# Optimization experiments

Hardware: AMD Instinct MI355X
Metric: run time of the kernel (lower is better)

The kernel has to match this reference:

```python
import jax, jax.numpy as jnp
import numpy as np

NVOC = 50257
DIM = 256
HID = 256
NUM_LAYERS = 2
SEQ = 128
BATCH = 16


def setup_inputs() -> dict:
    key = jax.random.key(0)
    ks = jax.random.split(key, 16)
    u = 0.1
    inp = {
        "tokens": jax.random.randint(ks[0], (SEQ, BATCH), 0, NVOC),
        "emb": jax.random.uniform(ks[1], (NVOC, DIM), jnp.float32, -u, u),
        # gate weights are zero-initialized nn.Parameters in the original; use small
        # random values so gradients/activations are non-degenerate
        "wf": jax.random.normal(ks[2], (HID, HID), jnp.float32) * 0.05,
        "uf": jax.random.normal(ks[3], (DIM, HID), jnp.float32) * 0.05,
        "bf": jnp.zeros((HID,), jnp.float32),
        "wi": jax.random.normal(ks[4], (HID, HID), jnp.float32) * 0.05,
        "ui": jax.random.normal(ks[5], (DIM, HID), jnp.float32) * 0.05,
        "bi": jnp.zeros((HID,), jnp.float32),
        "wc": jax.random.normal(ks[6], (HID, HID), jnp.float32) * 0.05,
        "uc": jax.random.normal(ks[7], (DIM, HID), jnp.float32) * 0.05,
        "bc": jnp.zeros((HID,), jnp.float32),
        "wo": jax.random.normal(ks[8], (HID, HID), jnp.float32) * 0.05,
        "uo": jax.random.normal(ks[9], (DIM, HID), jnp.float32) * 0.05,
        "bo": jnp.zeros((HID,), jnp.float32),
        "dec_w": jax.random.uniform(ks[10], (NVOC, HID), jnp.float32, -u, u),
        "dec_b": jnp.zeros((NVOC,), jnp.float32),
    }
    return inp


def reference(tokens, emb, wf, uf, bf, wi, ui, bi, wc, uc, bc, wo, uo, bo,
              dec_w, dec_b):
    # embeddings: (T, B, D); dropout is identity (eval / p honored as 0)
    x_seq = emb[tokens]

    h0 = jnp.zeros((NUM_LAYERS, BATCH, HID), jnp.float32)
    c0 = jnp.zeros((NUM_LAYERS, BATCH, HID), jnp.float32)

    def step(carry, x_t):
        h, c = carry
        x = x_t  # (B, D)
        hs, cs = [], []
        for l in range(NUM_LAYERS):  # fixed small structural loop
            hp, cp = h[l], c[l]
            f = jax.nn.sigmoid(hp @ wf + x @ uf + bf)
            i = jax.nn.sigmoid(hp @ wi + x @ ui + bi)
            o = jax.nn.sigmoid(hp @ wo + x @ uo + bo)
            g = jnp.tanh(hp @ wc + x @ uc + bc)
            cn = f * cp + i * g
            hn = o * jnp.tanh(cn)
            hs.append(hn)
            cs.append(cn)
            x = hn  # next layer consumes this layer's hidden state
        return (jnp.stack(hs), jnp.stack(cs)), x  # emit top-layer h

    (hT, cT), h_top = jax.lax.scan(step, (h0, c0), x_seq)  # h_top: (T, B, H)
    logits = jnp.einsum('tbh,vh->tbv', h_top, dec_w) + dec_b  # (T, B, V)
    return logits, hT, cT
```

## Files before the change

### kernel.cpp

```cpp
#include <hip/hip_runtime.h>
#include <hip/hip_bf16.h>

#define NVOC 50257
#define DIM 256
#define HID 256
#define NLAYER 2
#define SEQ 128
#define BATCH 16
#define GUARD (1 << 20)
#define NCHUNK 197
#define DECBLKS (32 * NCHUNK)
#define FL_L0 0
#define FL_XV 16
#define FL_L1 32
#define FSTR 64

typedef __bf16 bf16x8 __attribute__((ext_vector_type(8)));
typedef float f32x4 __attribute__((ext_vector_type(4)));
typedef unsigned short u16;
typedef unsigned int u32;
typedef unsigned long long u64;

#define AL64(p)   __hip_atomic_load((const u64*)(p), __ATOMIC_RELAXED, __HIP_MEMORY_SCOPE_AGENT)
#define AS32(p,v) __hip_atomic_store((u32*)(p), (v), __ATOMIC_RELAXED, __HIP_MEMORY_SCOPE_AGENT)

__device__ __forceinline__ float fsig(float z) { return 1.f / (1.f + __expf(-z)); }
__device__ __forceinline__ float ftanh(float z) {
  const float x = fminf(fmaxf(z, -15.f), 15.f);
  const float e = __expf(2.f * x);
  return (e - 1.f) / (e + 1.f);
}
__device__ __forceinline__ bf16x8 cvt8(const float4 u0, const float4 u1) {
  bf16x8 v;
  v[0] = (__bf16)u0.x; v[1] = (__bf16)u0.y; v[2] = (__bf16)u0.z; v[3] = (__bf16)u0.w;
  v[4] = (__bf16)u1.x; v[5] = (__bf16)u1.y; v[6] = (__bf16)u1.z; v[7] = (__bf16)u1.w;
  return v;
}

__device__ __forceinline__ bool all16(const u32* fp) {
  const u64 m = AL64(fp) & AL64(fp + 2) & AL64(fp + 4) & AL64(fp + 6)
              & AL64(fp + 8) & AL64(fp + 10) & AL64(fp + 12) & AL64(fp + 14);
  return ((u32)m & (u32)(m >> 32)) != 0u;
}
__device__ __forceinline__ void pollwave(const u32* fp, int lane) {
  if (lane == 0) {
    int gd = 0;
    while (!all16(fp) && ++gd < GUARD) {}
  }
  asm volatile("" ::: "memory");
}

__global__ void zero_kernel(u32* __restrict__ flg) {
  for (int i = threadIdx.x; i < SEQ * FSTR; i += 256) AS32(&flg[i], 0u);
}

__global__ __launch_bounds__(256) void xu_kernel(
    const int* __restrict__ tokp, const float* __restrict__ embp,
    const float* __restrict__ uF, const float* __restrict__ uI,
    const float* __restrict__ uC, const float* __restrict__ uO,
    const float* __restrict__ bF, const float* __restrict__ bI,
    const float* __restrict__ bC, const float* __restrict__ bO,
    float* __restrict__ XU)
{
  const int tid = threadIdx.x;
  const int lane = tid & 63, wv = tid >> 6, r16 = lane & 15, kgrp = lane >> 4;
  const int m0 = blockIdx.x * 16;
  const int n0 = blockIdx.y * 256 + wv * 64;
  const float* Ug[4] = {uF, uI, uC, uO};
  const float* Bp[4] = {bF, bI, bC, bO};

  bf16x8 b[4][8];
  float bias[4];
#pragma unroll
  for (int nt = 0; nt < 4; ++nt) {
    const int n = n0 + nt * 16 + r16;
    const float* U = Ug[n >> 8];
    const int c = n & 255;
    bias[nt] = Bp[n >> 8][c];
#pragma unroll
    for (int kk = 0; kk < 8; ++kk) {
      const int kb = kk * 32 + kgrp * 8;
      bf16x8 v;
#pragma unroll
      for (int e = 0; e < 8; ++e) v[e] = (__bf16)U[(size_t)(kb + e) * HID + c];
      b[nt][kk] = v;
    }
  }

  const int tok = tokp[m0 + r16];
  const float* x = embp + (size_t)tok * DIM;
  bf16x8 a[8];
#pragma unroll
  for (int kk = 0; kk < 8; ++kk) {
    const int kb = kk * 32 + kgrp * 8;
    a[kk] = cvt8(*reinterpret_cast<const float4*>(x + kb),
                 *reinterpret_cast<const float4*>(x + kb + 4));
  }
#pragma unroll
  for (int nt = 0; nt < 4; ++nt) {
    f32x4 acc = {0.f, 0.f, 0.f, 0.f};
#pragma unroll
    for (int kk = 0; kk < 8; ++kk)
      acc = __builtin_amdgcn_mfma_f32_16x16x32_bf16(a[kk], b[nt][kk], acc, 0, 0, 0);
    const int n = n0 + nt * 16 + r16;
#pragma unroll
    for (int r = 0; r < 4; ++r)
      XU[(size_t)(m0 + kgrp * 4 + r) * 1024 + n] = acc[r] + bias[nt];
  }
}

__global__ __launch_bounds__(512, 1) void mega_kernel(
    const float* __restrict__ wF, const float* __restrict__ wI,
    const float* __restrict__ wC, const float* __restrict__ wO,
    const float* __restrict__ uF, const float* __restrict__ uI,
    const float* __restrict__ uC, const float* __restrict__ uO,
    const float* __restrict__ bF, const float* __restrict__ bI,
    const float* __restrict__ bC, const float* __restrict__ bO,
    const float* __restrict__ XU, float* __restrict__ V,
    u32* __restrict__ h0w, u32* __restrict__ h1w,
    u32* __restrict__ flg, const float* __restrict__ dw,
    const float* __restrict__ dbp, float* __restrict__ dout)
{
  const int tid  = threadIdx.x;
  const int lane = tid & 63;
  const int wv   = tid >> 6;
  const int r16  = lane & 15;
  const int kgrp = lane >> 4;
  const int bx   = blockIdx.x;

  if (bx >= 6) {
    const int db = bx - 6;
    const int mb = db / NCHUNK;
    const int nb = db - mb * NCHUNK;
    const int n0 = nb * 256 + wv * 32;

    bf16x8 b[2][8];
    float bb[2];
#pragma unroll
    for (int nt = 0; nt < 2; ++nt) {
      const int v = n0 + nt * 16 + r16;
      const int vc = (v < NVOC) ? v : (NVOC - 1);
      bb[nt] = dbp[vc];
      const float* bp = dw + (size_t)vc * HID + kgrp * 8;
#pragma unroll
      for (int kk = 0; kk < 8; ++kk)
        b[nt][kk] = cvt8(*reinterpret_cast<const float4*>(bp + kk * 32),
                         *reinterpret_cast<const float4*>(bp + kk * 32 + 4));
    }

    if (tid == 0) {
      const u32* fp = flg + (size_t)(mb * 4 + 3) * FSTR + FL_L1;
      int gd = 0;
      while (!all16(fp) && ++gd < GUARD) __builtin_amdgcn_s_sleep(64);
    }
    __syncthreads();

    const u16* htb = (const u16*)h1w;
    bf16x8 a[4][8];
#pragma unroll
    for (int mt = 0; mt < 4; ++mt) {
      const u16* ap = htb + ((size_t)(mb * 64 + mt * 16 + r16)) * HID + kgrp * 8;
#pragma unroll
      for (int kk = 0; kk < 8; ++kk)
        a[mt][kk] = *reinterpret_cast<const bf16x8*>(ap + kk * 32);
    }

    f32x4 acc[4][2];
#pragma unroll
    for (int mt = 0; mt < 4; ++mt)
#pragma unroll
      for (int nt = 0; nt < 2; ++nt) {
        acc[mt][nt][0] = 0.f; acc[mt][nt][1] = 0.f;
        acc[mt][nt][2] = 0.f; acc[mt][nt][3] = 0.f;
      }
#pragma unroll
    for (int kk = 0; kk < 8; ++kk)
#pragma unroll
      for (int nt = 0; nt < 2; ++nt) {
        const bf16x8 bv = b[nt][kk];
#pragma unroll
        for (int mt = 0; mt < 4; ++mt)
          acc[mt][nt] = __builtin_amdgcn_mfma_f32_16x16x32_bf16(a[mt][kk], bv, acc[mt][nt], 0, 0, 0);
      }

#pragma unroll
    for (int nt = 0; nt < 2; ++nt) {
      const int v = n0 + nt * 16 + r16;
      if (v < NVOC) {
#pragma unroll
        for (int mt = 0; mt < 4; ++mt)
#pragma unroll
          for (int r = 0; r < 4; ++r)
            dout[(size_t)(mb * 64 + mt * 16 + kgrp * 4 + r) * NVOC + v] = acc[mt][nt][r] + bb[nt];
      }
    }
    return;
  }

  const int role = bx >> 1;
  const int wk   = (bx & 1) * 8 + wv;
  const float* Wg[4] = {wF, wI, wC, wO};
  const float* Ug[4] = {uF, uI, uC, uO};
  const float* Bg[4] = {bF, bI, bC, bO};
  const u16* h0s = (const u16*)h0w;
  const u16* h1s = (const u16*)h1w;
  const size_t logitsN = (size_t)SEQ * BATCH * NVOC;
  const int odd = lane & 1;

  if (role == 1) {
    bf16x8 u[4][8];
    float bias[4];
#pragma unroll
    for (int nt = 0; nt < 4; ++nt) {
      const int gcol = wk * 64 + nt * 16 + r16;
      const float* U = Ug[gcol >> 8];
      const int c = gcol & 255;
      bias[nt] = Bg[gcol >> 8][c];
#pragma unroll
      for (int kk = 0; kk < 8; ++kk) {
        const int kb = kk * 32 + kgrp * 8;
        bf16x8 v;
#pragma unroll
        for (int e = 0; e < 8; ++e) v[e] = (__bf16)U[(size_t)(kb + e) * HID + c];
        u[nt][kk] = v;
      }
    }

    for (int t = 0; t < SEQ; ++t) {
      pollwave(flg + (size_t)t * FSTR + FL_L0, lane);
      const u16* hp = h0s + ((size_t)t * BATCH + r16) * HID + kgrp * 8;
      bf16x8 hA[8];
#pragma unroll
      for (int kk = 0; kk < 8; ++kk)
        hA[kk] = *reinterpret_cast<const bf16x8*>(hp + kk * 32);

      f32x4 acc[4];
#pragma unroll
      for (int nt = 0; nt < 4; ++nt) { acc[nt][0]=0.f; acc[nt][1]=0.f; acc[nt][2]=0.f; acc[nt][3]=0.f; }
#pragma unroll
      for (int kk = 0; kk < 8; ++kk)
#pragma unroll
        for (int nt = 0; nt < 4; ++nt)
          acc[nt] = __builtin_amdgcn_mfma_f32_16x16x32_bf16(hA[kk], u[nt][kk], acc[nt], 0, 0, 0);

#pragma unroll
      for (int nt = 0; nt < 4; ++nt) {
        const int gcol = wk * 64 + nt * 16 + r16;
#pragma unroll
        for (int r = 0; r < 4; ++r)
          AS32((u32*)(V + ((size_t)(t * 16 + kgrp * 4 + r)) * 1024 + gcol),
               __builtin_bit_cast(u32, acc[nt][r] + bias[nt]));
      }
      asm volatile("s_waitcnt vmcnt(0)" ::: "memory");
      if (lane == 0) AS32(&flg[(size_t)t * FSTR + FL_XV + wk], 1u);
    }
    return;
  }

  const int col = wk * 16 + r16;
  bf16x8 wa[4][8];
#pragma unroll
  for (int g = 0; g < 4; ++g)
#pragma unroll
    for (int kk = 0; kk < 8; ++kk) {
      const int kb = kk * 32 + kgrp * 8;
      bf16x8 v;
#pragma unroll
      for (int e = 0; e < 8; ++e) v[e] = (__bf16)Wg[g][(size_t)(kb + e) * HID + col];
      wa[g][kk] = v;
    }

  float cst[4] = {0.f, 0.f, 0.f, 0.f};
  u32* hw = (role == 0) ? h0w : h1w;
  const u16* hs = (role == 0) ? h0s : h1s;
  const int flbase = (role == 0) ? FL_L0 : FL_L1;

  for (int t = 0; t < SEQ; ++t) {
    f32x4 acc[4];
#pragma unroll
    for (int g = 0; g < 4; ++g) { acc[g][0]=0.f; acc[g][1]=0.f; acc[g][2]=0.f; acc[g][3]=0.f; }

    if (t > 0) {
      pollwave(flg + (size_t)(t - 1) * FSTR + flbase, lane);
      const u16* hp = hs + ((size_t)(t - 1) * BATCH + r16) * HID + kgrp * 8;
      bf16x8 hA[8];
#pragma unroll
      for (int kk = 0; kk < 8; ++kk)
        hA[kk] = *reinterpret_cast<const bf16x8*>(hp + kk * 32);
#pragma unroll
      for (int kk = 0; kk < 8; ++kk)
#pragma unroll
        for (int g = 0; g < 4; ++g)
          acc[g] = __builtin_amdgcn_mfma_f32_16x16x32_bf16(hA[kk], wa[g][kk], acc[g], 0, 0, 0);
    }

    float xin[4][4];
    if (role == 0) {
#pragma unroll
      for (int g = 0; g < 4; ++g)
#pragma unroll
        for (int r = 0; r < 4; ++r)
          xin[g][r] = XU[(size_t)(t * 16 + kgrp * 4 + r) * 1024 + g * 256 + col];
    } else {
      pollwave(flg + (size_t)t * FSTR + FL_XV, lane);
#pragma unroll
      for (int g = 0; g < 4; ++g)
#pragma unroll
        for (int r = 0; r < 4; ++r)
          xin[g][r] = V[(size_t)(t * 16 + kgrp * 4 + r) * 1024 + g * 256 + col];
    }

    float hv[4];
#pragma unroll
    for (int r = 0; r < 4; ++r) {
      const float f = fsig(acc[0][r] + xin[0][r]);
      const float i = fsig(acc[1][r] + xin[1][r]);
      const float g = ftanh(acc[2][r] + xin[2][r]);
      const float o = fsig(acc[3][r] + xin[3][r]);
      cst[r] = f * cst[r] + i * g;
      hv[r] = o * ftanh(cst[r]);
    }
#pragma unroll
    for (int r = 0; r < 4; ++r) {
      const float ph = __shfl_xor(hv[r], 1);
      const u16 a = __builtin_bit_cast(u16, (__bf16)hv[r]);
      const u16 p = __builtin_bit_cast(u16, (__bf16)ph);
      const u32 pk = odd ? ((u32)p | ((u32)a << 16)) : ((u32)a | ((u32)p << 16));
      if ((r & 1) == odd)
        AS32(hw + ((size_t)t * BATCH + kgrp * 4 + r) * 128 + (col >> 1), pk);
    }
    if (t == SEQ - 1) {
      const int lb = (role == 0) ? 0 : BATCH;
#pragma unroll
      for (int r = 0; r < 4; ++r) {
        const int b = kgrp * 4 + r;
        dout[logitsN + (size_t)(lb + b) * HID + col] = hv[r];
        dout[logitsN + (size_t)NLAYER * BATCH * HID + (size_t)(lb + b) * HID + col] = cst[r];
      }
    }
    asm volatile("s_waitcnt vmcnt(0)" ::: "memory");
    if (lane == 0) AS32(&flg[(size_t)t * FSTR + flbase + wk], 1u);
  }
}

extern "C" void kernel_launch(void* const* d_in, const int* in_sizes, int n_in,
                              void* d_out, int out_size, void* d_ws, size_t ws_size,
                              hipStream_t stream) {
  const int*   tokp = (const int*)d_in[0];
  const float* embp = (const float*)d_in[1];
  const float* wF = (const float*)d_in[2];
  const float* uF = (const float*)d_in[3];
  const float* bF = (const float*)d_in[4];
  const float* wI = (const float*)d_in[5];
  const float* uI = (const float*)d_in[6];
  const float* bI = (const float*)d_in[7];
  const float* wC = (const float*)d_in[8];
  const float* uC = (const float*)d_in[9];
  const float* bC = (const float*)d_in[10];
  const float* wO = (const float*)d_in[11];
  const float* uO = (const float*)d_in[12];
  const float* bO = (const float*)d_in[13];
  const float* dw = (const float*)d_in[14];
  const float* db = (const float*)d_in[15];
  float* out = (float*)d_out;

  char* ws = (char*)d_ws;
  size_t off = 0;
  float* XU = (float*)(ws + off); off += (size_t)SEQ * BATCH * 1024 * 4;
  float* V  = (float*)(ws + off); off += (size_t)SEQ * BATCH * 1024 * 4;
  u32* h0w = (u32*)(ws + off); off += (size_t)SEQ * BATCH * HID * 2;
  u32* h1w = (u32*)(ws + off); off += (size_t)SEQ * BATCH * HID * 2;
  u32* flg = (u32*)(ws + off); off += (size_t)SEQ * FSTR * 4;

  zero_kernel<<<1, 256, 0, stream>>>(flg);
  xu_kernel<<<dim3(128, 4), 256, 0, stream>>>(tokp, embp, uF, uI, uC, uO,
                                              bF, bI, bC, bO, XU);
  mega_kernel<<<6 + DECBLKS, 512, 0, stream>>>(wF, wI, wC, wO, uF, uI, uC, uO,
                                               bF, bI, bC, bO, XU, V, h0w, h1w,
                                               flg, dw, db, out);
}
```

Baseline: 1.028 ms.

## Run each LSTM layer recurrence in a single block with LDS-exchanged hidden state

Each layer's recurrence now runs in one 256-thread block instead of two cooperating blocks. The hidden state moves through double-buffered LDS with a block barrier, replacing the global-memory flag polling between blocks. W weights sit partly in registers and partly in LDS. Two blocks compute layer-1 input projections ahead using 8 tiles per wave, and XU/V use a transposed layout so gate inputs load as vector-4 accumulator initial values. Decoder blocks now handle 64 columns per wave with a 4-row m-loop. The aim is to cut inter-block synchronisation latency on the serial critical path, at the cost of less parallelism per timestep and LDS loads in the inner loop.

Result: slower. 1.629 ms (+58.4%).

```diff
diff --git a/kernel.cpp b/kernel.cpp
--- a/kernel.cpp
+++ b/kernel.cpp
@@ -2,18 +2,20 @@
 #include <hip/hip_bf16.h>
 
 #define NVOC 50257
-#define DIM 256
 #define HID 256
 #define NLAYER 2
 #define SEQ 128
 #define BATCH 16
-#define GUARD (1 << 20)
+#define GUARD (1 << 18)
+#define DGUARD (1 << 15)
 #define NCHUNK 197
 #define DECBLKS (32 * NCHUNK)
-#define FL_L0 0
-#define FL_XV 16
-#define FL_L1 32
-#define FSTR 64
+#define FSTR 16
+#define REGK 6
+#define WLDS_BYTES (32 * 16 * 256)
+#define HROW 528
+#define HBUF (16 * HROW)
+#define SMEM_BYTES (WLDS_BYTES + 2 * HBUF)
 
 typedef __bf16 bf16x8 __attribute__((ext_vector_type(8)));
 typedef float f32x4 __attribute__((ext_vector_type(4)));
@@ -23,6 +25,7 @@
 
 #define AL64(p)   __hip_atomic_load((const u64*)(p), __ATOMIC_RELAXED, __HIP_MEMORY_SCOPE_AGENT)
 #define AS32(p,v) __hip_atomic_store((u32*)(p), (v), __ATOMIC_RELAXED, __HIP_MEMORY_SCOPE_AGENT)
+#define AS64(p,v) __hip_atomic_store((u64*)(p), (v), __ATOMIC_RELAXED, __HIP_MEMORY_SCOPE_AGENT)
 
 __device__ __forceinline__ float fsig(float z) { return 1.f / (1.f + __expf(-z)); }
 __device__ __forceinline__ float ftanh(float z) {
@@ -36,18 +39,24 @@
   v[4] = (__bf16)u1.x; v[5] = (__bf16)u1.y; v[6] = (__bf16)u1.z; v[7] = (__bf16)u1.w;
   return v;
 }
-
-__device__ __forceinline__ bool all16(const u32* fp) {
-  const u64 m = AL64(fp) & AL64(fp + 2) & AL64(fp + 4) & AL64(fp + 6)
-              & AL64(fp + 8) & AL64(fp + 10) & AL64(fp + 12) & AL64(fp + 14);
-  return ((u32)m & (u32)(m >> 32)) != 0u;
-}
-__device__ __forceinline__ void pollwave(const u32* fp, int lane) {
-  if (lane == 0) {
-    int gd = 0;
-    while (!all16(fp) && ++gd < GUARD) {}
-  }
-  asm volatile("" ::: "memory");
+__device__ __forceinline__ u64 pk64(float a, float b) {
+  return (u64)__builtin_bit_cast(u32, a) | ((u64)__builtin_bit_cast(u32, b) << 32);
+}
+__device__ __forceinline__ void poll4(const u32* fp) {
+  int gd = 0;
+  for (;;) {
+    const u64 m = AL64(fp) & AL64(fp + 2);
+    if (((u32)m & (u32)(m >> 32)) != 0u) break;
+    if (++gd >= GUARD) break;
+  }
+}
+__device__ __forceinline__ void poll8(const u32* fp) {
+  int gd = 0;
+  for (;;) {
+    const u64 m = AL64(fp) & AL64(fp + 2) & AL64(fp + 4) & AL64(fp + 6);
+    if (((u32)m & (u32)(m >> 32)) != 0u) break;
+    if (++gd >= GUARD) break;
+  }
 }
 
 __global__ void zero_kernel(u32* __restrict__ flg) {
@@ -64,7 +73,7 @@
 {
   const int tid = threadIdx.x;
   const int lane = tid & 63, wv = tid >> 6, r16 = lane & 15, kgrp = lane >> 4;
-  const int m0 = blockIdx.x * 16;
+  const int t  = blockIdx.x;
   const int n0 = blockIdx.y * 256 + wv * 64;
   const float* Ug[4] = {uF, uI, uC, uO};
   const float* Bp[4] = {bF, bI, bC, bO};
@@ -87,8 +96,8 @@
     }
   }
 
-  const int tok = tokp[m0 + r16];
-  const float* x = embp + (size_t)tok * DIM;
+  const int tok = tokp[t * BATCH + r16];
+  const float* x = embp + (size_t)tok * HID;
   bf16x8 a[8];
 #pragma unroll
   for (int kk = 0; kk < 8; ++kk) {
@@ -103,13 +112,14 @@
     for (int kk = 0; kk < 8; ++kk)
       acc = __builtin_amdgcn_mfma_f32_16x16x32_bf16(a[kk], b[nt][kk], acc, 0, 0, 0);
     const int n = n0 + nt * 16 + r16;
-#pragma unroll
-    for (int r = 0; r < 4; ++r)
-      XU[(size_t)(m0 + kgrp * 4 + r) * 1024 + n] = acc[r] + bias[nt];
-  }
-}
-
-__global__ __launch_bounds__(512, 1) void mega_kernel(
+    f32x4 st;
+#pragma unroll
+    for (int r = 0; r < 4; ++r) st[r] = acc[r] + bias[nt];
+    *reinterpret_cast<f32x4*>(XU + ((size_t)t * 1024 + n) * 16 + kgrp * 4) = st;
+  }
+}
+
+__global__ __launch_bounds__(256, 1) void mega_kernel(
     const float* __restrict__ wF, const float* __restrict__ wI,
     const float* __restrict__ wC, const float* __restrict__ wO,
     const float* __restrict__ uF, const float* __restrict__ uI,
@@ -121,23 +131,25 @@
     u32* __restrict__ flg, const float* __restrict__ dw,
     const float* __restrict__ dbp, float* __restrict__ dout)
 {
+  extern __shared__ char smem[];
   const int tid  = threadIdx.x;
   const int lane = tid & 63;
   const int wv   = tid >> 6;
   const int r16  = lane & 15;
   const int kgrp = lane >> 4;
   const int bx   = blockIdx.x;
-
-  if (bx >= 6) {
-    const int db = bx - 6;
+  const size_t logitsN = (size_t)SEQ * BATCH * NVOC;
+
+  if (bx >= 4) {
+    const int db = bx - 4;
     const int mb = db / NCHUNK;
     const int nb = db - mb * NCHUNK;
-    const int n0 = nb * 256 + wv * 32;
-
-    bf16x8 b[2][8];
-    float bb[2];
-#pragma unroll
-    for (int nt = 0; nt < 2; ++nt) {
+    const int n0 = nb * 256 + wv * 64;
+
+    bf16x8 b[4][8];
+    float bb[4];
+#pragma unroll
+    for (int nt = 0; nt < 4; ++nt) {
       const int v = n0 + nt * 16 + r16;
       const int vc = (v < NVOC) ? v : (NVOC - 1);
       bb[nt] = dbp[vc];
@@ -149,198 +161,240 @@
     }
 
     if (tid == 0) {
-      const u32* fp = flg + (size_t)(mb * 4 + 3) * FSTR + FL_L1;
+      const u32* fp = flg + (size_t)(mb * 4 + 3) * FSTR + 4;
       int gd = 0;
-      while (!all16(fp) && ++gd < GUARD) __builtin_amdgcn_s_sleep(64);
+      for (;;) {
+        const u64 m = AL64(fp) & AL64(fp + 2);
+        if (((u32)m & (u32)(m >> 32)) != 0u) break;
+        if (++gd >= DGUARD) break;
+        __builtin_amdgcn_s_sleep(64);
+      }
     }
     __syncthreads();
 
     const u16* htb = (const u16*)h1w;
-    bf16x8 a[4][8];
-#pragma unroll
+#pragma unroll 1
     for (int mt = 0; mt < 4; ++mt) {
-      const u16* ap = htb + ((size_t)(mb * 64 + mt * 16 + r16)) * HID + kgrp * 8;
-#pragma unroll
-      for (int kk = 0; kk < 8; ++kk)
-        a[mt][kk] = *reinterpret_cast<const bf16x8*>(ap + kk * 32);
-    }
-
-    f32x4 acc[4][2];
-#pragma unroll
-    for (int mt = 0; mt < 4; ++mt)
-#pragma unroll
-      for (int nt = 0; nt < 2; ++nt) {
-        acc[mt][nt][0] = 0.f; acc[mt][nt][1] = 0.f;
-        acc[mt][nt][2] = 0.f; acc[mt][nt][3] = 0.f;
-      }
-#pragma unroll
-    for (int kk = 0; kk < 8; ++kk)
-#pragma unroll
-      for (int nt = 0; nt < 2; ++nt) {
-        const bf16x8 bv = b[nt][kk];
-#pragma unroll
-        for (int mt = 0; mt < 4; ++mt)
-          acc[mt][nt] = __builtin_amdgcn_mfma_f32_16x16x32_bf16(a[mt][kk], bv, acc[mt][nt], 0, 0, 0);
-      }
-
-#pragma unroll
-    for (int nt = 0; nt < 2; ++nt) {
-      const int v = n0 + nt * 16 + r16;
-      if (v < NVOC) {
-#pragma unroll
-        for (int mt = 0; mt < 4; ++mt)
+      const int m = mb * 64 + mt * 16;
+      const u16* ap = htb + ((size_t)(m + r16)) * HID + kgrp * 8;
+      bf16x8 a[8];
+#pragma unroll
+      for (int kk = 0; kk < 8; ++kk)
+        a[kk] = *reinterpret_cast<const bf16x8*>(ap + kk * 32);
+      f32x4 acc[4];
+#pragma unroll
+      for (int nt = 0; nt < 4; ++nt) { acc[nt][0]=0.f; acc[nt][1]=0.f; acc[nt][2]=0.f; acc[nt][3]=0.f; }
+#pragma unroll
+      for (int kk = 0; kk < 8; ++kk)
+#pragma unroll
+        for (int nt = 0; nt < 4; ++nt)
+          acc[nt] = __builtin_amdgcn_mfma_f32_16x16x32_bf16(a[kk], b[nt][kk], acc[nt], 0, 0, 0);
+#pragma unroll
+      for (int nt = 0; nt < 4; ++nt) {
+        const int v = n0 + nt * 16 + r16;
+        if (v < NVOC) {
 #pragma unroll
           for (int r = 0; r < 4; ++r)
-            dout[(size_t)(mb * 64 + mt * 16 + kgrp * 4 + r) * NVOC + v] = acc[mt][nt][r] + bb[nt];
+            dout[(size_t)(m + kgrp * 4 + r) * NVOC + v] = acc[nt][r] + bb[nt];
+        }
       }
     }
     return;
   }
 
-  const int role = bx >> 1;
-  const int wk   = (bx & 1) * 8 + wv;
   const float* Wg[4] = {wF, wI, wC, wO};
   const float* Ug[4] = {uF, uI, uC, uO};
   const float* Bg[4] = {bF, bI, bC, bO};
-  const u16* h0s = (const u16*)h0w;
-  const u16* h1s = (const u16*)h1w;
-  const size_t logitsN = (size_t)SEQ * BATCH * NVOC;
-  const int odd = lane & 1;
-
-  if (role == 1) {
-    bf16x8 u[4][8];
-    float bias[4];
-#pragma unroll
-    for (int nt = 0; nt < 4; ++nt) {
-      const int gcol = wk * 64 + nt * 16 + r16;
+
+  if (bx == 1 || bx == 2) {
+    const int xb = bx - 1;
+    const int gbase = xb * 512 + wv * 128;
+    bf16x8 ureg[8][8];
+    float bias[8];
+#pragma unroll
+    for (int tile = 0; tile < 8; ++tile) {
+      const int gcol = gbase + tile * 16 + r16;
       const float* U = Ug[gcol >> 8];
       const int c = gcol & 255;
-      bias[nt] = Bg[gcol >> 8][c];
+      bias[tile] = Bg[gcol >> 8][c];
 #pragma unroll
       for (int kk = 0; kk < 8; ++kk) {
         const int kb = kk * 32 + kgrp * 8;
         bf16x8 v;
 #pragma unroll
         for (int e = 0; e < 8; ++e) v[e] = (__bf16)U[(size_t)(kb + e) * HID + c];
-        u[nt][kk] = v;
-      }
-    }
+        ureg[tile][kk] = v;
+      }
+    }
+    const u16* h0s = (const u16*)h0w;
+    const int myflag = 8 + xb * 4 + wv;
 
     for (int t = 0; t < SEQ; ++t) {
-      pollwave(flg + (size_t)t * FSTR + FL_L0, lane);
+      if (lane == 0) poll4(flg + (size_t)t * FSTR + 0);
+      asm volatile("" ::: "memory");
       const u16* hp = h0s + ((size_t)t * BATCH + r16) * HID + kgrp * 8;
       bf16x8 hA[8];
 #pragma unroll
       for (int kk = 0; kk < 8; ++kk)
         hA[kk] = *reinterpret_cast<const bf16x8*>(hp + kk * 32);
-
-      f32x4 acc[4];
-#pragma unroll
-      for (int nt = 0; nt < 4; ++nt) { acc[nt][0]=0.f; acc[nt][1]=0.f; acc[nt][2]=0.f; acc[nt][3]=0.f; }
-#pragma unroll
-      for (int kk = 0; kk < 8; ++kk)
-#pragma unroll
-        for (int nt = 0; nt < 4; ++nt)
-          acc[nt] = __builtin_amdgcn_mfma_f32_16x16x32_bf16(hA[kk], u[nt][kk], acc[nt], 0, 0, 0);
-
-#pragma unroll
-      for (int nt = 0; nt < 4; ++nt) {
-        const int gcol = wk * 64 + nt * 16 + r16;
-#pragma unroll
-        for (int r = 0; r < 4; ++r)
-          AS32((u32*)(V + ((size_t)(t * 16 + kgrp * 4 + r)) * 1024 + gcol),
-               __builtin_bit_cast(u32, acc[nt][r] + bias[nt]));
-      }
+      f32x4 acc[8];
+#pragma unroll
+      for (int tile = 0; tile < 8; ++tile) {
+        acc[tile][0] = bias[tile]; acc[tile][1] = bias[tile];
+        acc[tile][2] = bias[tile]; acc[tile][3] = bias[tile];
+      }
+#pragma unroll
+      for (int kk = 0; kk < 8; ++kk)
+#pragma unroll
+        for (int tile = 0; tile < 8; ++tile)
+          acc[tile] = __builtin_amdgcn_mfma_f32_16x16x32_bf16(hA[kk], ureg[tile][kk], acc[tile], 0, 0, 0);
       asm volatile("s_waitcnt vmcnt(0)" ::: "memory");
-      if (lane == 0) AS32(&flg[(size_t)t * FSTR + FL_XV + wk], 1u);
-    }
+      if (lane == 0 && t > 0) AS32(&flg[(size_t)(t - 1) * FSTR + myflag], 1u);
+#pragma unroll
+      for (int tile = 0; tile < 8; ++tile) {
+        const int gcol = gbase + tile * 16 + r16;
+        u64* vp = (u64*)(V + ((size_t)t * 1024 + gcol) * 16 + kgrp * 4);
+        AS64(vp,     pk64(acc[tile][0], acc[tile][1]));
+        AS64(vp + 1, pk64(acc[tile][2], acc[tile][3]));
+      }
+    }
+    asm volatile("s_waitcnt vmcnt(0)" ::: "memory");
+    if (lane == 0) AS32(&flg[(size_t)(SEQ - 1) * FSTR + myflag], 1u);
     return;
   }
 
-  const int col = wk * 16 + r16;
-  bf16x8 wa[4][8];
+  const int l = (bx == 3);
+  const float* xin = l ? V : XU;
+  u32* hw = l ? h1w : h0w;
+  const int flbase = l ? 4 : 0;
+
+  bf16x8 wreg[4][4][REGK];
 #pragma unroll
   for (int g = 0; g < 4; ++g)
 #pragma unroll
-    for (int kk = 0; kk < 8; ++kk) {
-      const int kb = kk * 32 + kgrp * 8;
-      bf16x8 v;
-#pragma unroll
-      for (int e = 0; e < 8; ++e) v[e] = (__bf16)Wg[g][(size_t)(kb + e) * HID + col];
-      wa[g][kk] = v;
-    }
-
-  float cst[4] = {0.f, 0.f, 0.f, 0.f};
-  u32* hw = (role == 0) ? h0w : h1w;
-  const u16* hs = (role == 0) ? h0s : h1s;
-  const int flbase = (role == 0) ? FL_L0 : FL_L1;
+    for (int ct = 0; ct < 4; ++ct) {
+      const int col = 64 * wv + ct * 16 + r16;
+#pragma unroll
+      for (int kk = 0; kk < 8; ++kk) {
+        const int kb = kk * 32 + kgrp * 8;
+        bf16x8 v;
+#pragma unroll
+        for (int e = 0; e < 8; ++e) v[e] = (__bf16)Wg[g][(size_t)(kb + e) * HID + col];
+        if (kk < REGK) {
+          wreg[g][ct][kk] = v;
+        } else {
+          const int lidx = (g * 4 + ct) * 2 + (kk - REGK);
+          *reinterpret_cast<bf16x8*>(smem + (((size_t)(wv * 32 + lidx) * 64 + lane) * 16)) = v;
+        }
+      }
+    }
+
+  float cst[4][4];
+#pragma unroll
+  for (int ct = 0; ct < 4; ++ct)
+#pragma unroll
+    for (int r = 0; r < 4; ++r) cst[ct][r] = 0.f;
+  const int odd = lane & 1;
 
   for (int t = 0; t < SEQ; ++t) {
-    f32x4 acc[4];
-#pragma unroll
-    for (int g = 0; g < 4; ++g) { acc[g][0]=0.f; acc[g][1]=0.f; acc[g][2]=0.f; acc[g][3]=0.f; }
-
+    asm volatile("s_waitcnt lgkmcnt(0)" ::: "memory");
+    __builtin_amdgcn_s_barrier();
+    __builtin_amdgcn_sched_barrier(0);
+
+    if (l) {
+      if (lane == 0) poll8(flg + (size_t)t * FSTR + 8);
+      asm volatile("" ::: "memory");
+    }
+
+    bf16x8 hA[8];
     if (t > 0) {
-      pollwave(flg + (size_t)(t - 1) * FSTR + flbase, lane);
-      const u16* hp = hs + ((size_t)(t - 1) * BATCH + r16) * HID + kgrp * 8;
-      bf16x8 hA[8];
-#pragma unroll
-      for (int kk = 0; kk < 8; ++kk)
-        hA[kk] = *reinterpret_cast<const bf16x8*>(hp + kk * 32);
-#pragma unroll
-      for (int kk = 0; kk < 8; ++kk)
-#pragma unroll
-        for (int g = 0; g < 4; ++g)
-          acc[g] = __builtin_amdgcn_mfma_f32_16x16x32_bf16(hA[kk], wa[g][kk], acc[g], 0, 0, 0);
-    }
-
-    float xin[4][4];
-    if (role == 0) {
+      const char* hbase = smem + WLDS_BYTES + ((t - 1) & 1) * HBUF + r16 * HROW + kgrp * 16;
+#pragma unroll
+      for (int kk = 0; kk < 8; ++kk)
+        hA[kk] = *reinterpret_cast<const bf16x8*>(hbase + kk * 64);
+    }
+
+    float hv[4][4];
+#pragma unroll
+    for (int hf2 = 0; hf2 < 2; ++hf2) {
+      f32x4 acc[4][2];
 #pragma unroll
       for (int g = 0; g < 4; ++g)
 #pragma unroll
-        for (int r = 0; r < 4; ++r)
-          xin[g][r] = XU[(size_t)(t * 16 + kgrp * 4 + r) * 1024 + g * 256 + col];
-    } else {
-      pollwave(flg + (size_t)t * FSTR + FL_XV, lane);
-#pragma unroll
-      for (int g = 0; g < 4; ++g)
-#pragma unroll
-        for (int r = 0; r < 4; ++r)
-          xin[g][r] = V[(size_t)(t * 16 + kgrp * 4 + r) * 1024 + g * 256 + col];
-    }
-
-    float hv[4];
-#pragma unroll
-    for (int r = 0; r < 4; ++r) {
-      const float f = fsig(acc[0][r] + xin[0][r]);
-      const float i = fsig(acc[1][r] + xin[1][r]);
-      const float g = ftanh(acc[2][r] + xin[2][r]);
-      const float o = fsig(acc[3][r] + xin[3][r]);
-      cst[r] = f * cst[r] + i * g;
-      hv[r] = o * ftanh(cst[r]);
-    }
-#pragma unroll
-    for (int r = 0; r < 4; ++r) {
-      const float ph = __shfl_xor(hv[r], 1);
-      const u16 a = __builtin_bit_cast(u16, (__bf16)hv[r]);
-      const u16 p = __builtin_bit_cast(u16, (__bf16)ph);
-      const u32 pk = odd ? ((u32)p | ((u32)a << 16)) : ((u32)a | ((u32)p << 16));
-      if ((r & 1) == odd)
-        AS32(hw + ((size_t)t * BATCH + kgrp * 4 + r) * 128 + (col >> 1), pk);
-    }
-    if (t == SEQ - 1) {
-      const int lb = (role == 0) ? 0 : BATCH;
-#pragma unroll
-      for (int r = 0; r < 4; ++r) {
-        const int b = kgrp * 4 + r;
-        dout[logitsN + (size_t)(lb + b) * HID + col] = hv[r];
-        dout[logitsN + (size_t)NLAYER * BATCH * HID + (size_t)(lb + b) * HID + col] = cst[r];
-      }
-    }
+        for (int c2 = 0; c2 < 2; ++c2) {
+          const int ct = hf2 * 2 + c2;
+          acc[g][c2] = *reinterpret_cast<const f32x4*>(
+              xin + ((size_t)t * 1024 + g * 256 + 64 * wv + ct * 16 + r16) * 16 + kgrp * 4);
+        }
+      if (t > 0) {
+#pragma unroll
+        for (int kk = 0; kk < REGK; ++kk)
+#pragma unroll
+          for (int g = 0; g < 4; ++g)
+#pragma unroll
+            for (int c2 = 0; c2 < 2; ++c2)
+              acc[g][c2] = __builtin_amdgcn_mfma_f32_16x16x32_bf16(
+                  hA[kk], wreg[g][hf2 * 2 + c2][kk], acc[g][c2], 0, 0, 0);
+#pragma unroll
+        for (int kk = REGK; kk < 8; ++kk)
+#pragma unroll
+          for (int g = 0; g < 4; ++g)
+#pragma unroll
+            for (int c2 = 0; c2 < 2; ++c2) {
+              const int lidx = (g * 4 + (hf2 * 2 + c2)) * 2 + (kk - REGK);
+              const bf16x8 wt = *reinterpret_cast<const bf16x8*>(
+                  smem + (((size_t)(wv * 32 + lidx) * 64 + lane) * 16));
+              acc[g][c2] = __builtin_amdgcn_mfma_f32_16x16x32_bf16(hA[kk], wt, acc[g][c2], 0, 0, 0);
+            }
+      }
+#pragma unroll
+      for (int c2 = 0; c2 < 2; ++c2) {
+        const int ct = hf2 * 2 + c2;
+#pragma unroll
+        for (int r = 0; r < 4; ++r) {
+          const float f = fsig(acc[0][c2][r]);
+          const float i = fsig(acc[1][c2][r]);
+          const float g = ftanh(acc[2][c2][r]);
+          const float o = fsig(acc[3][c2][r]);
+          cst[ct][r] = f * cst[ct][r] + i * g;
+          hv[ct][r] = o * ftanh(cst[ct][r]);
+        }
+      }
+    }
+
     asm volatile("s_waitcnt vmcnt(0)" ::: "memory");
-    if (lane == 0) AS32(&flg[(size_t)t * FSTR + flbase + wk], 1u);
-  }
+    if (t > 0 && lane == 0) AS32(&flg[(size_t)(t - 1) * FSTR + flbase + wv], 1u);
+
+    {
+      char* hdst = smem + WLDS_BYTES + (t & 1) * HBUF;
+#pragma unroll
+      for (int ct = 0; ct < 4; ++ct)
+#pragma unroll
+        for (int r = 0; r < 4; ++r) {
+          const int col = 64 * wv + ct * 16 + r16;
+          const u16 hb = __builtin_bit_cast(u16, (__bf16)hv[ct][r]);
+          *reinterpret_cast<u16*>(hdst + (kgrp * 4 + r) * HROW + col * 2) = hb;
+          const float ph = __shfl_xor(hv[ct][r], 1);
+          const u16 pb = __builtin_bit_cast(u16, (__bf16)ph);
+          const u32 pk = odd ? ((u32)pb | ((u32)hb << 16)) : ((u32)hb | ((u32)pb << 16));
+          if ((r & 1) == odd)
+            AS32(hw + ((size_t)t * BATCH + kgrp * 4 + r) * 128 + (col >> 1), pk);
+        }
+      if (t == SEQ - 1) {
+#pragma unroll
+        for (int ct = 0; ct < 4; ++ct)
+#pragma unroll
+          for (int r = 0; r < 4; ++r) {
+            const int col = 64 * wv + ct * 16 + r16;
+            const int b = kgrp * 4 + r;
+            dout[logitsN + (size_t)(l * BATCH + b) * HID + col] = hv[ct][r];
+            dout[logitsN + (size_t)NLAYER * BATCH * HID + (size_t)(l * BATCH + b) * HID + col] = cst[ct][r];
+          }
+      }
+    }
+  }
+  asm volatile("s_waitcnt vmcnt(0)" ::: "memory");
+  if (lane == 0) AS32(&flg[(size_t)(SEQ - 1) * FSTR + flbase + wv], 1u);
 }
 
 extern "C" void kernel_launch(void* const* d_in, const int* in_sizes, int n_in,
@@ -366,16 +420,16 @@
 
   char* ws = (char*)d_ws;
   size_t off = 0;
-  float* XU = (float*)(ws + off); off += (size_t)SEQ * BATCH * 1024 * 4;
-  float* V  = (float*)(ws + off); off += (size_t)SEQ * BATCH * 1024 * 4;
+  float* XU = (float*)(ws + off); off += (size_t)SEQ * 1024 * BATCH * 4;
+  float* V  = (float*)(ws + off); off += (size_t)SEQ * 1024 * BATCH * 4;
   u32* h0w = (u32*)(ws + off); off += (size_t)SEQ * BATCH * HID * 2;
   u32* h1w = (u32*)(ws + off); off += (size_t)SEQ * BATCH * HID * 2;
   u32* flg = (u32*)(ws + off); off += (size_t)SEQ * FSTR * 4;
 
   zero_kernel<<<1, 256, 0, stream>>>(flg);
-  xu_kernel<<<dim3(128, 4), 256, 0, stream>>>(tokp, embp, uF, uI, uC, uO,
+  xu_kernel<<<dim3(SEQ, 4), 256, 0, stream>>>(tokp, embp, uF, uI, uC, uO,
                                               bF, bI, bC, bO, XU);
-  mega_kernel<<<6 + DECBLKS, 512, 0, stream>>>(wF, wI, wC, wO, uF, uI, uC, uO,
-                                               bF, bI, bC, bO, XU, V, h0w, h1w,
-                                               flg, dw, db, out);
-}
+  mega_kernel<<<4 + DECBLKS, 256, SMEM_BYTES, stream>>>(
+      wF, wI, wC, wO, uF, uI, uC, uO, bF, bI, bC, bO,
+      XU, V, h0w, h1w, flg, dw, db, out);
+}
```
